# Performance work log

Measured on AMD Instinct MI355X. Metric: run time of the kernel, lower is better.

The kernel has to match this reference:

```python
import jax, jax.numpy as jnp
import numpy as np
import math

N_HEADS = 16
ROPE_BASE = 10000.0


def _rope_interleaved(t, cos, sin):
    # t: [B,H,T,dk]; cos/sin: [T, dk//2] broadcast over B,H
    te, to = t[..., 0::2], t[..., 1::2]
    re = te * cos - to * sin
    ro = te * sin + to * cos
    # interleave back: [..., dk//2, 2] -> [..., dk]
    return jnp.stack([re, ro], axis=-1).reshape(t.shape)


def setup_inputs() -> dict:
    key = jax.random.key(0)
    ks = jax.random.split(key, 5)
    B, T, C = 2, 2048, 1024
    s = 1.0 / math.sqrt(C)
    return {
        "x": jax.random.normal(ks[0], (B, T, C), dtype=jnp.float32),
        "W_qkv": jax.random.normal(ks[1], (C, 3 * C), dtype=jnp.float32) * s,
        "b_qkv": jax.random.normal(ks[2], (3 * C,), dtype=jnp.float32) * 0.02,
        "W_proj": jax.random.normal(ks[3], (C, C), dtype=jnp.float32) * s,
        "b_proj": jax.random.normal(ks[4], (C,), dtype=jnp.float32) * 0.02,
    }


def reference(x, W_qkv, b_qkv, W_proj, b_proj):
    B, T, C = x.shape
    H = N_HEADS
    dk = C // H

    qkv = x @ W_qkv + b_qkv                      # [B,T,3C]
    q, k, v = jnp.split(qkv, 3, axis=-1)
    q = q.reshape(B, T, H, dk).transpose(0, 2, 1, 3)  # [B,H,T,dk]
    k = k.reshape(B, T, H, dk).transpose(0, 2, 1, 3)
    v = v.reshape(B, T, H, dk).transpose(0, 2, 1, 3)

    # RoPE angles: pos * base^(-2i/dk)
    freqs = ROPE_BASE ** (-2.0 * jnp.arange(dk // 2, dtype=jnp.float32) / dk)
    angles = jnp.arange(T, dtype=jnp.float32)[:, None] * freqs[None, :]  # [T,dk//2]
    cos, sin = jnp.cos(angles), jnp.sin(angles)

    q = _rope_interleaved(q, cos, sin)
    k = _rope_interleaved(k, cos, sin)

    attn = jnp.einsum("bhqd,bhkd->bhqk", q, k) / math.sqrt(dk)  # [B,H,T,T]
    causal = jnp.triu(jnp.full((T, T), -jnp.inf, dtype=attn.dtype), k=1)
    attn = jax.nn.softmax(attn + causal, axis=-1)

    scores = jnp.einsum("bhqk,bhkd->bhqd", attn, v)  # [B,H,T,dk]
    scores = scores.transpose(0, 2, 1, 3).reshape(B, T, C)
    return scores @ W_proj + b_proj
```

## Files before the change

### kernel.cpp

```cpp
#include <hip/hip_runtime.h>
#include <hip/hip_bf16.h>

typedef __bf16 bf16x8 __attribute__((ext_vector_type(8)));
typedef float f32x4 __attribute__((ext_vector_type(4)));
typedef float f32x16 __attribute__((ext_vector_type(16)));
typedef unsigned short u16;
typedef u16 u16x8 __attribute__((ext_vector_type(8)));

__device__ __forceinline__ u16 f2bf(float f) {
  union { float f; unsigned u; } v; v.f = f;
  unsigned r = v.u + 0x7fffu + ((v.u >> 16) & 1u);
  return (u16)(r >> 16);
}
__device__ __forceinline__ float bf2f(u16 u) {
  union { unsigned u; float f; } v; v.u = (unsigned)u << 16; return v.f;
}
__device__ __forceinline__ unsigned cvtpk(float a, float b) {
  unsigned r;
  asm("v_cvt_pk_bf16_f32 %0, %1, %2" : "=v"(r) : "v"(a), "v"(b));
  return r;
}
__device__ __forceinline__ float exp2_(float x) {
  float r;
  asm("v_exp_f32 %0, %1" : "=v"(r) : "v"(x));
  return r;
}
__device__ __forceinline__ float sin2pi_(float x) {
  float r;
  asm("v_sin_f32 %0, %1" : "=v"(r) : "v"(x));
  return r;
}
__device__ __forceinline__ float cos2pi_(float x) {
  float r;
  asm("v_cos_f32 %0, %1" : "=v"(r) : "v"(x));
  return r;
}
__device__ __forceinline__ void gload16(const void* g, void* l) {
  __builtin_amdgcn_global_load_lds(
      (__attribute__((address_space(1))) void*)(void*)g,
      (__attribute__((address_space(3))) void*)l, 16, 0, 0);
}

union U8 { bf16x8 v; unsigned u[4]; };

__global__ __launch_bounds__(256) void cast_x_k(const float* __restrict__ x,
                                                u16* __restrict__ xb, int n8) {
  int id = blockIdx.x * 256 + threadIdx.x;
  if (id >= n8) return;
  const float4* p = (const float4*)(x + (size_t)id * 8);
  float4 a = p[0], b = p[1];
  u16x8 o;
  o[0] = f2bf(a.x); o[1] = f2bf(a.y); o[2] = f2bf(a.z); o[3] = f2bf(a.w);
  o[4] = f2bf(b.x); o[5] = f2bf(b.y); o[6] = f2bf(b.z); o[7] = f2bf(b.w);
  *(u16x8*)(xb + (size_t)id * 8) = o;
}

__global__ __launch_bounds__(256) void tcast_k(const float* __restrict__ W,
                                               u16* __restrict__ Wt, int R, int Cc) {
  __shared__ float tile[32][33];
  int bx = blockIdx.x * 32, by = blockIdx.y * 32;
  int tx = threadIdx.x & 31, ty = threadIdx.x >> 5;
#pragma unroll
  for (int j = 0; j < 4; j++)
    tile[ty + j * 8][tx] = W[(size_t)(by + ty + j * 8) * Cc + bx + tx];
  __syncthreads();
#pragma unroll
  for (int j = 0; j < 4; j++)
    Wt[(size_t)(bx + ty + j * 8) * R + by + tx] = f2bf(tile[tx][ty + j * 8]);
}

template <bool BF16OUT>
__global__ __launch_bounds__(256) void gemm_bt_k(const u16* __restrict__ A,
                                                 const u16* __restrict__ Bt,
                                                 const float* __restrict__ bias,
                                                 void* __restrict__ Cv,
                                                 int M, int N, int K) {
  __shared__ u16 As[128 * 64];
  __shared__ u16 Bs[128 * 64];
  int tid = threadIdx.x;
  int m0 = blockIdx.y * 128, n0 = blockIdx.x * 128;
  int wave = tid >> 6, lane = tid & 63;
  int wm = (wave & 1) * 64, wn = (wave >> 1) * 64;
  int lrow = lane & 15, lk = (lane >> 4) * 8;
  int rr = lane >> 3, cb = (lane & 7) * 16;

  f32x4 acc[4][4] = {};

  for (int k0 = 0; k0 < K; k0 += 64) {
#pragma unroll
    for (int i = 0; i < 4; i++) {
      int row = wave * 32 + i * 8 + rr;
      int cc = (cb ^ ((row & 7) << 4)) >> 1;
      gload16(A + (size_t)(m0 + row) * K + k0 + cc, &As[(wave * 32 + i * 8) * 64]);
      gload16(Bt + (size_t)(n0 + row) * K + k0 + cc, &Bs[(wave * 32 + i * 8) * 64]);
    }
    __syncthreads();
#pragma unroll
    for (int kk = 0; kk < 2; kk++) {
      bf16x8 af[4], bfr[4];
#pragma unroll
      for (int i = 0; i < 4; i++) {
        int arow = wm + i * 16 + lrow;
        int ab = (arow * 128 + (kk * 32 + lk) * 2) ^ ((arow & 7) << 4);
        af[i] = *(const bf16x8*)((const char*)As + ab);
        int brow = wn + i * 16 + lrow;
        int bb = (brow * 128 + (kk * 32 + lk) * 2) ^ ((brow & 7) << 4);
        bfr[i] = *(const bf16x8*)((const char*)Bs + bb);
      }
#pragma unroll
      for (int i = 0; i < 4; i++)
#pragma unroll
        for (int j = 0; j < 4; j++)
          acc[i][j] = __builtin_amdgcn_mfma_f32_16x16x32_bf16(af[i], bfr[j], acc[i][j], 0, 0, 0);
    }
    __syncthreads();
  }
  int rg = lane >> 4;
#pragma unroll
  for (int i = 0; i < 4; i++) {
#pragma unroll
    for (int j = 0; j < 4; j++) {
      int col = n0 + wn + j * 16 + lrow;
      float bz = bias ? bias[col] : 0.f;
#pragma unroll
      for (int r = 0; r < 4; r++) {
        int row = m0 + wm + i * 16 + rg * 4 + r;
        float val = acc[i][j][r] + bz;
        if constexpr (BF16OUT)
          ((u16*)Cv)[(size_t)row * N + col] = f2bf(val);
        else
          ((float*)Cv)[(size_t)row * N + col] = val;
      }
    }
  }
}

__global__ __launch_bounds__(256) void rope_pack_k(const u16* __restrict__ qkv,
                                                   u16* __restrict__ qf,
                                                   u16* __restrict__ kf,
                                                   u16* __restrict__ vf) {
  __shared__ u16 tl[64][72];
  int bh = blockIdx.x, tb = blockIdx.y;
  int b = bh >> 4, h = bh & 15;
  int tid = threadIdx.x;
  int tloc = tid >> 2;
  int a = tid & 3;
  int tg = tb * 64 + tloc;
  const u16* rowp = qkv + ((size_t)(b * 2048 + tg)) * 3072 + h * 64 + 16 * a;
  u16x8 q0 = *(const u16x8*)(rowp);
  u16x8 q1 = *(const u16x8*)(rowp + 8);
  u16x8 k0 = *(const u16x8*)(rowp + 1024);
  u16x8 k1 = *(const u16x8*)(rowp + 1032);
  const float QS = 0.18033688011112042f;
  const float C1 = -0.41524101186092029f;
  const float C2 = 0.15915494309189535f;
  u16x8 qo0, qo1, ko0, ko1;
#pragma unroll
  for (int j = 0; j < 8; j++) {
    int i = 8 * a + j;
    float fr = (float)tg * (exp2f((float)i * C1) * C2);
    fr = fr - floorf(fr);
    float sv = sin2pi_(fr), cv = cos2pi_(fr);
    float qx, qy, kx, ky;
    if (j < 4) {
      qx = bf2f(q0[2 * j]); qy = bf2f(q0[2 * j + 1]);
      kx = bf2f(k0[2 * j]); ky = bf2f(k0[2 * j + 1]);
    } else {
      qx = bf2f(q1[2 * j - 8]); qy = bf2f(q1[2 * j - 7]);
      kx = bf2f(k1[2 * j - 8]); ky = bf2f(k1[2 * j - 7]);
    }
    u16 qre = f2bf((qx * cv - qy * sv) * QS), qro = f2bf((qx * sv + qy * cv) * QS);
    u16 kre = f2bf(kx * cv - ky * sv),        kro = f2bf(kx * sv + ky * cv);
    if (j < 4) { qo0[2 * j] = qre; qo0[2 * j + 1] = qro; ko0[2 * j] = kre; ko0[2 * j + 1] = kro; }
    else       { qo1[2 * j - 8] = qre; qo1[2 * j - 7] = qro; ko1[2 * j - 8] = kre; ko1[2 * j - 7] = kro; }
  }
  size_t qbase = ((size_t)bh * 64 + (tg >> 5)) * 2048 + a * 512 + (tg & 31) * 8;
  *(u16x8*)(qf + qbase) = qo0;
  *(u16x8*)(qf + qbase + 256) = qo1;
  size_t kbase = (((size_t)bh * 32 + (tg >> 6)) * 2 + ((tg >> 5) & 1)) * 2048 + a * 512 + (tg & 31) * 8;
  *(u16x8*)(kf + kbase) = ko0;
  *(u16x8*)(kf + kbase + 256) = ko1;
#pragma unroll
  for (int rep = 0; rep < 2; rep++) {
    int tr = rep * 32 + (tid >> 3);
    int dc = (tid & 7) * 8;
    u16x8 v = *(const u16x8*)(qkv + ((size_t)(b * 2048 + tb * 64 + tr)) * 3072 + 2048 + h * 64 + dc);
    *(u16x8*)&tl[tr][dc] = v;
  }
  __syncthreads();
  u16* dst = vf + ((size_t)bh * 32 + tb) * 4096;
#pragma unroll
  for (int rep = 0; rep < 2; rep++) {
    int c = rep * 256 + tid;
    int dh = c >> 8, s = (c >> 6) & 3, l = c & 63;
    int hi = l >> 5, ql = l & 31;
    u16x8 o;
#pragma unroll
    for (int j = 0; j < 8; j++) o[j] = tl[s * 16 + hi * 8 + j][dh * 32 + ql];
    *(u16x8*)(dst + (size_t)c * 8) = o;
  }
}


#define KPREF(K0, K1, IT)                                                         \
  do {                                                                            \
    const u16* kb_ = KfP + (size_t)(IT) * 4096 + ln8;                             \
    _Pragma("unroll") for (int d_ = 0; d_ < 4; d_++) {                            \
      K0[d_] = *(const bf16x8*)(kb_ + d_ * 512);                                  \
      K1[d_] = *(const bf16x8*)(kb_ + 2048 + d_ * 512);                           \
    }                                                                             \
  } while (0)

#define QKC(SA, SB, K0, K1)                                                       \
  do {                                                                            \
    SA = (f32x16){};                                                              \
    SB = (f32x16){};                                                              \
    _Pragma("unroll") for (int d_ = 0; d_ < 4; d_++) {                            \
      SA = __builtin_amdgcn_mfma_f32_32x32x16_bf16(K0[d_], qfr[d_], SA, 0, 0, 0); \
      SB = __builtin_amdgcn_mfma_f32_32x32x16_bf16(K1[d_], qfr[d_], SB, 0, 0, 0); \
    }                                                                             \
  } while (0)

#define VLOADM(IT)                                                                \
  do {                                                                            \
    const u16* vb_ = VfP + (size_t)(IT) * 4096 + ln8;                             \
    _Pragma("unroll") for (int s_ = 0; s_ < 4; s_++) {                            \
      vv0[s_] = *(const bf16x8*)(vb_ + s_ * 512);                                 \
      vv1[s_] = *(const bf16x8*)(vb_ + 2048 + s_ * 512);                          \
    }                                                                             \
  } while (0)

#define SMPV(SA, SB, IT, MASKF)                                                   \
  do {                                                                            \
    if (MASKF) {                                                                  \
      int kv0_ = (IT) * 64;                                                       \
      _Pragma("unroll") for (int r_ = 0; r_ < 16; r_++) {                         \
        int ro_ = (r_ & 3) + 8 * (r_ >> 2) + 4 * hi;                              \
        if (kv0_ + ro_ > qg) SA[r_] = -3e38f;                                     \
        if (kv0_ + 32 + ro_ > qg) SB[r_] = -3e38f;                                \
      }                                                                           \
    }                                                                             \
    _Pragma("unroll") for (int r_ = 0; r_ < 16; r_++) {                           \
      SA[r_] = exp2_(SA[r_]);                                                     \
      SB[r_] = exp2_(SB[r_]);                                                     \
    }                                                                             \
    unsigned w0_ = cvtpk(SA[0], SA[1]),   w1_ = cvtpk(SA[2], SA[3]);              \
    unsigned w2_ = cvtpk(SA[4], SA[5]),   w3_ = cvtpk(SA[6], SA[7]);              \
    unsigned w4_ = cvtpk(SA[8], SA[9]),   w5_ = cvtpk(SA[10], SA[11]);            \
    unsigned w6_ = cvtpk(SA[12], SA[13]), w7_ = cvtpk(SA[14], SA[15]);            \
    unsigned y0_ = cvtpk(SB[0], SB[1]),   y1_ = cvtpk(SB[2], SB[3]);              \
    unsigned y2_ = cvtpk(SB[4], SB[5]),   y3_ = cvtpk(SB[6], SB[7]);              \
    unsigned y4_ = cvtpk(SB[8], SB[9]),   y5_ = cvtpk(SB[10], SB[11]);            \
    unsigned y6_ = cvtpk(SB[12], SB[13]), y7_ = cvtpk(SB[14], SB[15]);            \
    asm("v_permlane32_swap_b32 %0, %1" : "+v"(w0_), "+v"(w2_));                   \
    asm("v_permlane32_swap_b32 %0, %1" : "+v"(w1_), "+v"(w3_));                   \
    asm("v_permlane32_swap_b32 %0, %1" : "+v"(w4_), "+v"(w6_));                   \
    asm("v_permlane32_swap_b32 %0, %1" : "+v"(w5_), "+v"(w7_));                   \
    asm("v_permlane32_swap_b32 %0, %1" : "+v"(y0_), "+v"(y2_));                   \
    asm("v_permlane32_swap_b32 %0, %1" : "+v"(y1_), "+v"(y3_));                   \
    asm("v_permlane32_swap_b32 %0, %1" : "+v"(y4_), "+v"(y6_));                   \
    asm("v_permlane32_swap_b32 %0, %1" : "+v"(y5_), "+v"(y7_));                   \
    U8 pf0_, pf1_, pf2_, pf3_;                                                    \
    pf0_.u[0] = w0_; pf0_.u[1] = w1_; pf0_.u[2] = w2_; pf0_.u[3] = w3_;           \
    pf1_.u[0] = w4_; pf1_.u[1] = w5_; pf1_.u[2] = w6_; pf1_.u[3] = w7_;           \
    pf2_.u[0] = y0_; pf2_.u[1] = y1_; pf2_.u[2] = y2_; pf2_.u[3] = y3_;           \
    pf3_.u[0] = y4_; pf3_.u[1] = y5_; pf3_.u[2] = y6_; pf3_.u[3] = y7_;           \
    o0 = __builtin_amdgcn_mfma_f32_32x32x16_bf16(vv0[0], pf0_.v, o0, 0, 0, 0);    \
    o1 = __builtin_amdgcn_mfma_f32_32x32x16_bf16(vv1[0], pf0_.v, o1, 0, 0, 0);    \
    o0 = __builtin_amdgcn_mfma_f32_32x32x16_bf16(vv0[1], pf1_.v, o0, 0, 0, 0);    \
    o1 = __builtin_amdgcn_mfma_f32_32x32x16_bf16(vv1[1], pf1_.v, o1, 0, 0, 0);    \
    o0 = __builtin_amdgcn_mfma_f32_32x32x16_bf16(vv0[2], pf2_.v, o0, 0, 0, 0);    \
    o1 = __builtin_amdgcn_mfma_f32_32x32x16_bf16(vv1[2], pf2_.v, o1, 0, 0, 0);    \
    o0 = __builtin_amdgcn_mfma_f32_32x32x16_bf16(vv0[3], pf3_.v, o0, 0, 0, 0);    \
    o1 = __builtin_amdgcn_mfma_f32_32x32x16_bf16(vv1[3], pf3_.v, o1, 0, 0, 0);    \
    ls = __builtin_amdgcn_mfma_f32_32x32x16_bf16(onesf.v, pf0_.v, ls, 0, 0, 0);   \
    ls = __builtin_amdgcn_mfma_f32_32x32x16_bf16(onesf.v, pf1_.v, ls, 0, 0, 0);   \
    ls = __builtin_amdgcn_mfma_f32_32x32x16_bf16(onesf.v, pf2_.v, ls, 0, 0, 0);   \
    ls = __builtin_amdgcn_mfma_f32_32x32x16_bf16(onesf.v, pf3_.v, ls, 0, 0, 0);   \
  } while (0)

__global__ __launch_bounds__(64) void attn_k(const u16* __restrict__ Qf,
                                             const u16* __restrict__ Kf,
                                             const u16* __restrict__ Vf,
                                             u16* __restrict__ pO,
                                             float* __restrict__ pL) {
  const int T = 2048;
  int blk = blockIdx.x;
  int bh = (blk & 7) * 4 + ((blk >> 3) & 3);
  int c = blk >> 5;
  int qt, slot;
  if (c < 128)      { qt = 32 + (c >> 2);        slot = c & 3; }
  else if (c < 160) { qt = 16 + ((c - 128) >> 1); slot = (c - 128) & 1; }
  else              { qt = c - 160;               slot = 0; }
  int nTot = (qt >> 1) + 1;
  int nslots = (qt < 16) ? 1 : (qt < 32 ? 2 : 4);
  int it0 = (nTot * slot) / nslots;
  int itEnd = (nTot * (slot + 1)) / nslots;
  int lane = threadIdx.x & 63;
  int ql = lane & 31, hi = lane >> 5;
  int ln8 = lane * 8;
  int qg = qt * 32 + ql;
  const u16* QfP = Qf + (size_t)bh * 64 * 2048;
  const u16* KfP = Kf + (size_t)bh * 32 * 4096;
  const u16* VfP = Vf + (size_t)bh * 32 * 4096;
  int b = bh >> 4, h = bh & 15;

  U8 onesf;
#pragma unroll
  for (int j = 0; j < 4; j++) onesf.u[j] = 0x3F803F80u;

  bf16x8 qfr[4];
#pragma unroll
  for (int ds = 0; ds < 4; ds++)
    qfr[ds] = *(const bf16x8*)(QfP + (size_t)qt * 2048 + ds * 512 + ln8);

  f32x16 o0 = {}, o1 = {}, ls = {};
  bf16x8 Ka0[4], Ka1[4], Kb0[4], Kb1[4], vv0[4], vv1[4];
  f32x16 sA0, sA1, sB0, sB1;

  int t = it0;
  KPREF(Ka0, Ka1, t);
  QKC(sA0, sA1, Ka0, Ka1);
  if (t + 1 < itEnd) KPREF(Kb0, Kb1, t + 1);

  for (;;) {
    bool last = (t == itEnd - 1);
    VLOADM(t);
    if (t + 2 < itEnd) KPREF(Ka0, Ka1, t + 2);
    if (!last) QKC(sB0, sB1, Kb0, Kb1);
    SMPV(sA0, sA1, t, t == nTot - 1);
    if (last) break;
    ++t;
    last = (t == itEnd - 1);
    VLOADM(t);
    if (t + 2 < itEnd) KPREF(Kb0, Kb1, t + 2);
    if (!last) QKC(sA0, sA1, Ka0, Ka1);
    SMPV(sB0, sB1, t, t == nTot - 1);
    if (last) break;
    ++t;
  }

  u16* orow = pO + (size_t)slot * 4194304 + ((size_t)(b * T + qg)) * 1024 + h * 64;
#pragma unroll
  for (int j = 0; j < 4; j++) {
    ushort4 o;
    o.x = f2bf(o0[4 * j + 0]); o.y = f2bf(o0[4 * j + 1]);
    o.z = f2bf(o0[4 * j + 2]); o.w = f2bf(o0[4 * j + 3]);
    *(ushort4*)(orow + 8 * j + 4 * hi) = o;
    ushort4 q2;
    q2.x = f2bf(o1[4 * j + 0]); q2.y = f2bf(o1[4 * j + 1]);
    q2.z = f2bf(o1[4 * j + 2]); q2.w = f2bf(o1[4 * j + 3]);
    *(ushort4*)(orow + 32 + 8 * j + 4 * hi) = q2;
  }
  if (hi == 0) pL[slot * 65536 + bh * 2048 + qg] = ls[0];
}

__global__ __launch_bounds__(256) void mrg_k(const u16* __restrict__ pO,
                                             const float* __restrict__ pL,
                                             u16* __restrict__ sc) {
  int id = blockIdx.x * 256 + threadIdx.x;
  int col8 = id & 127;
  int row = id >> 7;
  int t = row & 2047, b = row >> 11;
  int h = col8 >> 3;
  int qt = t >> 5;
  int ns = (qt < 16) ? 1 : (qt < 32 ? 2 : 4);
  int bh = b * 16 + h;
  float acc[8] = {};
  float lsum = 0.f;
  for (int s = 0; s < ns; s++) {
    lsum += pL[s * 65536 + bh * 2048 + t];
    u16x8 v = *(const u16x8*)(pO + (size_t)s * 4194304 + (size_t)id * 8);
#pragma unroll
    for (int j = 0; j < 8; j++) acc[j] += bf2f(v[j]);
  }
  float inv = 1.f / lsum;
  u16x8 o;
#pragma unroll
  for (int j = 0; j < 8; j++) o[j] = f2bf(acc[j] * inv);
  *(u16x8*)(sc + (size_t)id * 8) = o;
}

extern "C" void kernel_launch(void* const* d_in, const int* in_sizes, int n_in,
                              void* d_out, int out_size, void* d_ws, size_t ws_size,
                              hipStream_t stream) {
  const float* x      = (const float*)d_in[0];
  const float* W_qkv  = (const float*)d_in[1];
  const float* b_qkv  = (const float*)d_in[2];
  const float* W_proj = (const float*)d_in[3];
  const float* b_proj = (const float*)d_in[4];
  float* out = (float*)d_out;

  const int B = 2, T = 2048, C = 1024;
  const int M = B * T;

  char* ws = (char*)d_ws;
  u16* wprojt = (u16*)(ws);
  u16* xb     = (u16*)(ws + (2ull << 20));
  u16* wqkvt  = (u16*)(ws + (10ull << 20));
  u16* qkvb   = (u16*)(ws + (16ull << 20));
  u16* pO     = (u16*)(ws + (2ull << 20));
  float* pL   = (float*)(ws + (34ull << 20));
  u16* qfb    = (u16*)(ws + (40ull << 20));
  u16* kfb    = (u16*)(ws + (48ull << 20));
  u16* vfb    = (u16*)(ws + (56ull << 20));
  u16* sc     = (u16*)(ws + (64ull << 20));

  cast_x_k<<<(M * C / 8 + 255) / 256, 256, 0, stream>>>(x, xb, M * C / 8);
  tcast_k<<<dim3(3 * C / 32, C / 32), 256, 0, stream>>>(W_qkv, wqkvt, C, 3 * C);
  tcast_k<<<dim3(C / 32, C / 32), 256, 0, stream>>>(W_proj, wprojt, C, C);
  gemm_bt_k<true><<<dim3(3 * C / 128, M / 128), 256, 0, stream>>>(xb, wqkvt, b_qkv, qkvb, M, 3 * C, C);
  rope_pack_k<<<dim3(B * 16, T / 64), 256, 0, stream>>>(qkvb, qfb, kfb, vfb);
  attn_k<<<5632, 64, 0, stream>>>(qfb, kfb, vfb, pO, pL);
  mrg_k<<<M * C / 8 / 256, 256, 0, stream>>>(pO, pL, sc);
  gemm_bt_k<false><<<dim3(C / 128, M / 128), 256, 0, stream>>>(sc, wprojt, b_proj, out, M, C, C);
}
```

Baseline: 130.0 us.

## Use 32-key attention tiles, rebalance split-K slots, skip merge for unsplit rows

The attention kernel now walks the causal range in 32-key steps instead of 64-key steps, which cuts masked wasted work on the diagonal. It redistributes query tiles across 4, 3, 2 or 1 split slots to balance per-block work, with a 5120-block grid. Blocks that are not split normalize and write straight to the score buffer, so the merge kernel only handles the split rows (t >= 512). In exchange it drops the double-buffered K prefetch and the overlap of QK and PV across iterations, relying on the occupancy hint (launch_bounds 64,4) to hide load latency instead.

```diff
diff --git a/kernel.cpp b/kernel.cpp
--- a/kernel.cpp
+++ b/kernel.cpp
@@ -201,107 +201,30 @@
   }
 }
 
-
-#define KPREF(K0, K1, IT)                                                         \
-  do {                                                                            \
-    const u16* kb_ = KfP + (size_t)(IT) * 4096 + ln8;                             \
-    _Pragma("unroll") for (int d_ = 0; d_ < 4; d_++) {                            \
-      K0[d_] = *(const bf16x8*)(kb_ + d_ * 512);                                  \
-      K1[d_] = *(const bf16x8*)(kb_ + 2048 + d_ * 512);                           \
-    }                                                                             \
-  } while (0)
-
-#define QKC(SA, SB, K0, K1)                                                       \
-  do {                                                                            \
-    SA = (f32x16){};                                                              \
-    SB = (f32x16){};                                                              \
-    _Pragma("unroll") for (int d_ = 0; d_ < 4; d_++) {                            \
-      SA = __builtin_amdgcn_mfma_f32_32x32x16_bf16(K0[d_], qfr[d_], SA, 0, 0, 0); \
-      SB = __builtin_amdgcn_mfma_f32_32x32x16_bf16(K1[d_], qfr[d_], SB, 0, 0, 0); \
-    }                                                                             \
-  } while (0)
-
-#define VLOADM(IT)                                                                \
-  do {                                                                            \
-    const u16* vb_ = VfP + (size_t)(IT) * 4096 + ln8;                             \
-    _Pragma("unroll") for (int s_ = 0; s_ < 4; s_++) {                            \
-      vv0[s_] = *(const bf16x8*)(vb_ + s_ * 512);                                 \
-      vv1[s_] = *(const bf16x8*)(vb_ + 2048 + s_ * 512);                          \
-    }                                                                             \
-  } while (0)
-
-#define SMPV(SA, SB, IT, MASKF)                                                   \
-  do {                                                                            \
-    if (MASKF) {                                                                  \
-      int kv0_ = (IT) * 64;                                                       \
-      _Pragma("unroll") for (int r_ = 0; r_ < 16; r_++) {                         \
-        int ro_ = (r_ & 3) + 8 * (r_ >> 2) + 4 * hi;                              \
-        if (kv0_ + ro_ > qg) SA[r_] = -3e38f;                                     \
-        if (kv0_ + 32 + ro_ > qg) SB[r_] = -3e38f;                                \
-      }                                                                           \
-    }                                                                             \
-    _Pragma("unroll") for (int r_ = 0; r_ < 16; r_++) {                           \
-      SA[r_] = exp2_(SA[r_]);                                                     \
-      SB[r_] = exp2_(SB[r_]);                                                     \
-    }                                                                             \
-    unsigned w0_ = cvtpk(SA[0], SA[1]),   w1_ = cvtpk(SA[2], SA[3]);              \
-    unsigned w2_ = cvtpk(SA[4], SA[5]),   w3_ = cvtpk(SA[6], SA[7]);              \
-    unsigned w4_ = cvtpk(SA[8], SA[9]),   w5_ = cvtpk(SA[10], SA[11]);            \
-    unsigned w6_ = cvtpk(SA[12], SA[13]), w7_ = cvtpk(SA[14], SA[15]);            \
-    unsigned y0_ = cvtpk(SB[0], SB[1]),   y1_ = cvtpk(SB[2], SB[3]);              \
-    unsigned y2_ = cvtpk(SB[4], SB[5]),   y3_ = cvtpk(SB[6], SB[7]);              \
-    unsigned y4_ = cvtpk(SB[8], SB[9]),   y5_ = cvtpk(SB[10], SB[11]);            \
-    unsigned y6_ = cvtpk(SB[12], SB[13]), y7_ = cvtpk(SB[14], SB[15]);            \
-    asm("v_permlane32_swap_b32 %0, %1" : "+v"(w0_), "+v"(w2_));                   \
-    asm("v_permlane32_swap_b32 %0, %1" : "+v"(w1_), "+v"(w3_));                   \
-    asm("v_permlane32_swap_b32 %0, %1" : "+v"(w4_), "+v"(w6_));                   \
-    asm("v_permlane32_swap_b32 %0, %1" : "+v"(w5_), "+v"(w7_));                   \
-    asm("v_permlane32_swap_b32 %0, %1" : "+v"(y0_), "+v"(y2_));                   \
-    asm("v_permlane32_swap_b32 %0, %1" : "+v"(y1_), "+v"(y3_));                   \
-    asm("v_permlane32_swap_b32 %0, %1" : "+v"(y4_), "+v"(y6_));                   \
-    asm("v_permlane32_swap_b32 %0, %1" : "+v"(y5_), "+v"(y7_));                   \
-    U8 pf0_, pf1_, pf2_, pf3_;                                                    \
-    pf0_.u[0] = w0_; pf0_.u[1] = w1_; pf0_.u[2] = w2_; pf0_.u[3] = w3_;           \
-    pf1_.u[0] = w4_; pf1_.u[1] = w5_; pf1_.u[2] = w6_; pf1_.u[3] = w7_;           \
-    pf2_.u[0] = y0_; pf2_.u[1] = y1_; pf2_.u[2] = y2_; pf2_.u[3] = y3_;           \
-    pf3_.u[0] = y4_; pf3_.u[1] = y5_; pf3_.u[2] = y6_; pf3_.u[3] = y7_;           \
-    o0 = __builtin_amdgcn_mfma_f32_32x32x16_bf16(vv0[0], pf0_.v, o0, 0, 0, 0);    \
-    o1 = __builtin_amdgcn_mfma_f32_32x32x16_bf16(vv1[0], pf0_.v, o1, 0, 0, 0);    \
-    o0 = __builtin_amdgcn_mfma_f32_32x32x16_bf16(vv0[1], pf1_.v, o0, 0, 0, 0);    \
-    o1 = __builtin_amdgcn_mfma_f32_32x32x16_bf16(vv1[1], pf1_.v, o1, 0, 0, 0);    \
-    o0 = __builtin_amdgcn_mfma_f32_32x32x16_bf16(vv0[2], pf2_.v, o0, 0, 0, 0);    \
-    o1 = __builtin_amdgcn_mfma_f32_32x32x16_bf16(vv1[2], pf2_.v, o1, 0, 0, 0);    \
-    o0 = __builtin_amdgcn_mfma_f32_32x32x16_bf16(vv0[3], pf3_.v, o0, 0, 0, 0);    \
-    o1 = __builtin_amdgcn_mfma_f32_32x32x16_bf16(vv1[3], pf3_.v, o1, 0, 0, 0);    \
-    ls = __builtin_amdgcn_mfma_f32_32x32x16_bf16(onesf.v, pf0_.v, ls, 0, 0, 0);   \
-    ls = __builtin_amdgcn_mfma_f32_32x32x16_bf16(onesf.v, pf1_.v, ls, 0, 0, 0);   \
-    ls = __builtin_amdgcn_mfma_f32_32x32x16_bf16(onesf.v, pf2_.v, ls, 0, 0, 0);   \
-    ls = __builtin_amdgcn_mfma_f32_32x32x16_bf16(onesf.v, pf3_.v, ls, 0, 0, 0);   \
-  } while (0)
-
-__global__ __launch_bounds__(64) void attn_k(const u16* __restrict__ Qf,
-                                             const u16* __restrict__ Kf,
-                                             const u16* __restrict__ Vf,
-                                             u16* __restrict__ pO,
-                                             float* __restrict__ pL) {
+__global__ __launch_bounds__(64, 4) void attn_k(const u16* __restrict__ Qf,
+                                                const u16* __restrict__ Kf,
+                                                const u16* __restrict__ Vf,
+                                                u16* __restrict__ sc,
+                                                u16* __restrict__ pO,
+                                                float* __restrict__ pL) {
   const int T = 2048;
   int blk = blockIdx.x;
   int bh = (blk & 7) * 4 + ((blk >> 3) & 3);
   int c = blk >> 5;
-  int qt, slot;
-  if (c < 128)      { qt = 32 + (c >> 2);        slot = c & 3; }
-  else if (c < 160) { qt = 16 + ((c - 128) >> 1); slot = (c - 128) & 1; }
-  else              { qt = c - 160;               slot = 0; }
-  int nTot = (qt >> 1) + 1;
-  int nslots = (qt < 16) ? 1 : (qt < 32 ? 2 : 4);
-  int it0 = (nTot * slot) / nslots;
-  int itEnd = (nTot * (slot + 1)) / nslots;
+  int qt, slot, nslots;
+  if (c < 64)       { qt = 63 - (c >> 2);              slot = c & 3;        nslots = 4; }
+  else if (c < 112) { int cc = c - 64; int d3 = cc / 3; qt = 47 - d3;       slot = cc - 3 * d3; nslots = 3; }
+  else if (c < 144) { int cc = c - 112; qt = 31 - (cc >> 1); slot = cc & 1; nslots = 2; }
+  else              { qt = 159 - c;                    slot = 0;            nslots = 1; }
+  int nIter = qt + 1;
+  int it0 = (nIter * slot) / nslots;
+  int itEnd = (nIter * (slot + 1)) / nslots;
   int lane = threadIdx.x & 63;
   int ql = lane & 31, hi = lane >> 5;
   int ln8 = lane * 8;
   int qg = qt * 32 + ql;
   const u16* QfP = Qf + (size_t)bh * 64 * 2048;
-  const u16* KfP = Kf + (size_t)bh * 32 * 4096;
+  const u16* KfP = Kf + (size_t)bh * 64 * 2048;
   const u16* VfP = Vf + (size_t)bh * 32 * 4096;
   int b = bh >> 4, h = bh & 15;
 
@@ -315,44 +238,81 @@
     qfr[ds] = *(const bf16x8*)(QfP + (size_t)qt * 2048 + ds * 512 + ln8);
 
   f32x16 o0 = {}, o1 = {}, ls = {};
-  bf16x8 Ka0[4], Ka1[4], Kb0[4], Kb1[4], vv0[4], vv1[4];
-  f32x16 sA0, sA1, sB0, sB1;
-
-  int t = it0;
-  KPREF(Ka0, Ka1, t);
-  QKC(sA0, sA1, Ka0, Ka1);
-  if (t + 1 < itEnd) KPREF(Kb0, Kb1, t + 1);
-
-  for (;;) {
-    bool last = (t == itEnd - 1);
-    VLOADM(t);
-    if (t + 2 < itEnd) KPREF(Ka0, Ka1, t + 2);
-    if (!last) QKC(sB0, sB1, Kb0, Kb1);
-    SMPV(sA0, sA1, t, t == nTot - 1);
-    if (last) break;
-    ++t;
-    last = (t == itEnd - 1);
-    VLOADM(t);
-    if (t + 2 < itEnd) KPREF(Kb0, Kb1, t + 2);
-    if (!last) QKC(sA0, sA1, Ka0, Ka1);
-    SMPV(sB0, sB1, t, t == nTot - 1);
-    if (last) break;
-    ++t;
-  }
-
-  u16* orow = pO + (size_t)slot * 4194304 + ((size_t)(b * T + qg)) * 1024 + h * 64;
-#pragma unroll
-  for (int j = 0; j < 4; j++) {
-    ushort4 o;
-    o.x = f2bf(o0[4 * j + 0]); o.y = f2bf(o0[4 * j + 1]);
-    o.z = f2bf(o0[4 * j + 2]); o.w = f2bf(o0[4 * j + 3]);
-    *(ushort4*)(orow + 8 * j + 4 * hi) = o;
-    ushort4 q2;
-    q2.x = f2bf(o1[4 * j + 0]); q2.y = f2bf(o1[4 * j + 1]);
-    q2.z = f2bf(o1[4 * j + 2]); q2.w = f2bf(o1[4 * j + 3]);
-    *(ushort4*)(orow + 32 + 8 * j + 4 * hi) = q2;
-  }
-  if (hi == 0) pL[slot * 65536 + bh * 2048 + qg] = ls[0];
+
+  for (int t = it0; t < itEnd; ++t) {
+    const u16* kb = KfP + (size_t)t * 2048 + ln8;
+    bf16x8 k0 = *(const bf16x8*)(kb);
+    bf16x8 k1 = *(const bf16x8*)(kb + 512);
+    bf16x8 k2 = *(const bf16x8*)(kb + 1024);
+    bf16x8 k3 = *(const bf16x8*)(kb + 1536);
+    f32x16 S = {};
+    S = __builtin_amdgcn_mfma_f32_32x32x16_bf16(k0, qfr[0], S, 0, 0, 0);
+    S = __builtin_amdgcn_mfma_f32_32x32x16_bf16(k1, qfr[1], S, 0, 0, 0);
+    S = __builtin_amdgcn_mfma_f32_32x32x16_bf16(k2, qfr[2], S, 0, 0, 0);
+    S = __builtin_amdgcn_mfma_f32_32x32x16_bf16(k3, qfr[3], S, 0, 0, 0);
+    const u16* vb = VfP + (size_t)(t >> 1) * 4096 + (t & 1) * 1024 + ln8;
+    bf16x8 v00 = *(const bf16x8*)(vb);
+    bf16x8 v01 = *(const bf16x8*)(vb + 512);
+    bf16x8 v10 = *(const bf16x8*)(vb + 2048);
+    bf16x8 v11 = *(const bf16x8*)(vb + 2560);
+    if (t == nIter - 1) {
+      int kv0 = t * 32;
+#pragma unroll
+      for (int r = 0; r < 16; r++) {
+        int k = kv0 + ((r & 3) + 8 * (r >> 2) + 4 * hi);
+        if (k > qg) S[r] = -3e38f;
+      }
+    }
+#pragma unroll
+    for (int r = 0; r < 16; r++) S[r] = exp2_(S[r]);
+    unsigned w0 = cvtpk(S[0], S[1]),   w1 = cvtpk(S[2], S[3]);
+    unsigned w2 = cvtpk(S[4], S[5]),   w3 = cvtpk(S[6], S[7]);
+    unsigned w4 = cvtpk(S[8], S[9]),   w5 = cvtpk(S[10], S[11]);
+    unsigned w6 = cvtpk(S[12], S[13]), w7 = cvtpk(S[14], S[15]);
+    asm("v_permlane32_swap_b32 %0, %1" : "+v"(w0), "+v"(w2));
+    asm("v_permlane32_swap_b32 %0, %1" : "+v"(w1), "+v"(w3));
+    asm("v_permlane32_swap_b32 %0, %1" : "+v"(w4), "+v"(w6));
+    asm("v_permlane32_swap_b32 %0, %1" : "+v"(w5), "+v"(w7));
+    U8 pf0, pf1;
+    pf0.u[0] = w0; pf0.u[1] = w1; pf0.u[2] = w2; pf0.u[3] = w3;
+    pf1.u[0] = w4; pf1.u[1] = w5; pf1.u[2] = w6; pf1.u[3] = w7;
+    o0 = __builtin_amdgcn_mfma_f32_32x32x16_bf16(v00, pf0.v, o0, 0, 0, 0);
+    o0 = __builtin_amdgcn_mfma_f32_32x32x16_bf16(v01, pf1.v, o0, 0, 0, 0);
+    o1 = __builtin_amdgcn_mfma_f32_32x32x16_bf16(v10, pf0.v, o1, 0, 0, 0);
+    o1 = __builtin_amdgcn_mfma_f32_32x32x16_bf16(v11, pf1.v, o1, 0, 0, 0);
+    ls = __builtin_amdgcn_mfma_f32_32x32x16_bf16(onesf.v, pf0.v, ls, 0, 0, 0);
+    ls = __builtin_amdgcn_mfma_f32_32x32x16_bf16(onesf.v, pf1.v, ls, 0, 0, 0);
+  }
+
+  if (nslots == 1) {
+    float inv = 1.f / ls[0];
+    u16* orow = sc + ((size_t)(b * T + qg)) * 1024 + h * 64;
+#pragma unroll
+    for (int j = 0; j < 4; j++) {
+      ushort4 o;
+      o.x = f2bf(o0[4 * j + 0] * inv); o.y = f2bf(o0[4 * j + 1] * inv);
+      o.z = f2bf(o0[4 * j + 2] * inv); o.w = f2bf(o0[4 * j + 3] * inv);
+      *(ushort4*)(orow + 8 * j + 4 * hi) = o;
+      ushort4 q2;
+      q2.x = f2bf(o1[4 * j + 0] * inv); q2.y = f2bf(o1[4 * j + 1] * inv);
+      q2.z = f2bf(o1[4 * j + 2] * inv); q2.w = f2bf(o1[4 * j + 3] * inv);
+      *(ushort4*)(orow + 32 + 8 * j + 4 * hi) = q2;
+    }
+  } else {
+    u16* orow = pO + (size_t)slot * 4194304 + ((size_t)(b * T + qg)) * 1024 + h * 64;
+#pragma unroll
+    for (int j = 0; j < 4; j++) {
+      ushort4 o;
+      o.x = f2bf(o0[4 * j + 0]); o.y = f2bf(o0[4 * j + 1]);
+      o.z = f2bf(o0[4 * j + 2]); o.w = f2bf(o0[4 * j + 3]);
+      *(ushort4*)(orow + 8 * j + 4 * hi) = o;
+      ushort4 q2;
+      q2.x = f2bf(o1[4 * j + 0]); q2.y = f2bf(o1[4 * j + 1]);
+      q2.z = f2bf(o1[4 * j + 2]); q2.w = f2bf(o1[4 * j + 3]);
+      *(ushort4*)(orow + 32 + 8 * j + 4 * hi) = q2;
+    }
+    if (hi == 0) pL[slot * 65536 + bh * 2048 + qg] = ls[0];
+  }
 }
 
 __global__ __launch_bounds__(256) void mrg_k(const u16* __restrict__ pO,
@@ -360,17 +320,19 @@
                                              u16* __restrict__ sc) {
   int id = blockIdx.x * 256 + threadIdx.x;
   int col8 = id & 127;
-  int row = id >> 7;
-  int t = row & 2047, b = row >> 11;
+  int rp = id >> 7;
+  int b = (rp >= 1536) ? 1 : 0;
+  int t = 512 + rp - b * 1536;
   int h = col8 >> 3;
   int qt = t >> 5;
-  int ns = (qt < 16) ? 1 : (qt < 32 ? 2 : 4);
+  int ns = (qt >= 48) ? 4 : (qt >= 32) ? 3 : 2;
   int bh = b * 16 + h;
+  size_t idx8 = ((size_t)(b * 2048 + t) * 128 + col8);
   float acc[8] = {};
   float lsum = 0.f;
   for (int s = 0; s < ns; s++) {
     lsum += pL[s * 65536 + bh * 2048 + t];
-    u16x8 v = *(const u16x8*)(pO + (size_t)s * 4194304 + (size_t)id * 8);
+    u16x8 v = *(const u16x8*)(pO + (size_t)s * 4194304 + idx8 * 8);
 #pragma unroll
     for (int j = 0; j < 8; j++) acc[j] += bf2f(v[j]);
   }
@@ -378,7 +340,7 @@
   u16x8 o;
 #pragma unroll
   for (int j = 0; j < 8; j++) o[j] = f2bf(acc[j] * inv);
-  *(u16x8*)(sc + (size_t)id * 8) = o;
+  *(u16x8*)(sc + idx8 * 8) = o;
 }
 
 extern "C" void kernel_launch(void* const* d_in, const int* in_sizes, int n_in,
@@ -411,7 +373,7 @@
   tcast_k<<<dim3(C / 32, C / 32), 256, 0, stream>>>(W_proj, wprojt, C, C);
   gemm_bt_k<true><<<dim3(3 * C / 128, M / 128), 256, 0, stream>>>(xb, wqkvt, b_qkv, qkvb, M, 3 * C, C);
   rope_pack_k<<<dim3(B * 16, T / 64), 256, 0, stream>>>(qkvb, qfb, kfb, vfb);
-  attn_k<<<5632, 64, 0, stream>>>(qfb, kfb, vfb, pO, pL);
-  mrg_k<<<M * C / 8 / 256, 256, 0, stream>>>(pO, pL, sc);
+  attn_k<<<5120, 64, 0, stream>>>(qfb, kfb, vfb, sc, pO, pL);
+  mrg_k<<<1536, 256, 0, stream>>>(pO, pL, sc);
   gemm_bt_k<false><<<dim3(C / 128, M / 128), 256, 0, stream>>>(sc, wprojt, b_proj, out, M, C, C);
 }
```

Result: faster. 121.2 us (-6.8%).

## Reduce attention split-K to two slots for late tiles and normalize in-kernel

Applied to the files above, without the earlier changes.

Changes the attention work split so only the last 16 query tiles (qt 48-63) are split into two KV slots, and all other tiles run unsplit, longest tiles first. Unsplit tiles now normalize by the row sum and write final bf16 output directly, so the merge kernel only runs over the 512 rows per batch that were split. This cuts partial-output traffic and merge work and shrinks the grid from 5632 to 2560 blocks. In exchange there is less parallelism, and long unsplit tiles in the middle range may leave the tail of the launch unbalanced.

```diff
diff --git a/kernel.cpp b/kernel.cpp
--- a/kernel.cpp
+++ b/kernel.cpp
@@ -282,18 +282,17 @@
 __global__ __launch_bounds__(64) void attn_k(const u16* __restrict__ Qf,
                                              const u16* __restrict__ Kf,
                                              const u16* __restrict__ Vf,
+                                             u16* __restrict__ sc,
                                              u16* __restrict__ pO,
                                              float* __restrict__ pL) {
   const int T = 2048;
   int blk = blockIdx.x;
   int bh = (blk & 7) * 4 + ((blk >> 3) & 3);
   int c = blk >> 5;
-  int qt, slot;
-  if (c < 128)      { qt = 32 + (c >> 2);        slot = c & 3; }
-  else if (c < 160) { qt = 16 + ((c - 128) >> 1); slot = (c - 128) & 1; }
-  else              { qt = c - 160;               slot = 0; }
+  int qt, slot, nslots;
+  if (c < 32) { qt = 63 - (c >> 1); slot = c & 1; nslots = 2; }
+  else        { qt = 79 - c;        slot = 0;     nslots = 1; }
   int nTot = (qt >> 1) + 1;
-  int nslots = (qt < 16) ? 1 : (qt < 32 ? 2 : 4);
   int it0 = (nTot * slot) / nslots;
   int itEnd = (nTot * (slot + 1)) / nslots;
   int lane = threadIdx.x & 63;
@@ -340,19 +339,35 @@
     ++t;
   }
 
-  u16* orow = pO + (size_t)slot * 4194304 + ((size_t)(b * T + qg)) * 1024 + h * 64;
-#pragma unroll
-  for (int j = 0; j < 4; j++) {
-    ushort4 o;
-    o.x = f2bf(o0[4 * j + 0]); o.y = f2bf(o0[4 * j + 1]);
-    o.z = f2bf(o0[4 * j + 2]); o.w = f2bf(o0[4 * j + 3]);
-    *(ushort4*)(orow + 8 * j + 4 * hi) = o;
-    ushort4 q2;
-    q2.x = f2bf(o1[4 * j + 0]); q2.y = f2bf(o1[4 * j + 1]);
-    q2.z = f2bf(o1[4 * j + 2]); q2.w = f2bf(o1[4 * j + 3]);
-    *(ushort4*)(orow + 32 + 8 * j + 4 * hi) = q2;
-  }
-  if (hi == 0) pL[slot * 65536 + bh * 2048 + qg] = ls[0];
+  if (nslots == 1) {
+    float inv = 1.f / ls[0];
+    u16* orow = sc + ((size_t)(b * T + qg)) * 1024 + h * 64;
+#pragma unroll
+    for (int j = 0; j < 4; j++) {
+      ushort4 o;
+      o.x = f2bf(o0[4 * j + 0] * inv); o.y = f2bf(o0[4 * j + 1] * inv);
+      o.z = f2bf(o0[4 * j + 2] * inv); o.w = f2bf(o0[4 * j + 3] * inv);
+      *(ushort4*)(orow + 8 * j + 4 * hi) = o;
+      ushort4 q2;
+      q2.x = f2bf(o1[4 * j + 0] * inv); q2.y = f2bf(o1[4 * j + 1] * inv);
+      q2.z = f2bf(o1[4 * j + 2] * inv); q2.w = f2bf(o1[4 * j + 3] * inv);
+      *(ushort4*)(orow + 32 + 8 * j + 4 * hi) = q2;
+    }
+  } else {
+    u16* orow = pO + (size_t)slot * 4194304 + ((size_t)(b * T + qg)) * 1024 + h * 64;
+#pragma unroll
+    for (int j = 0; j < 4; j++) {
+      ushort4 o;
+      o.x = f2bf(o0[4 * j + 0]); o.y = f2bf(o0[4 * j + 1]);
+      o.z = f2bf(o0[4 * j + 2]); o.w = f2bf(o0[4 * j + 3]);
+      *(ushort4*)(orow + 8 * j + 4 * hi) = o;
+      ushort4 q2;
+      q2.x = f2bf(o1[4 * j + 0]); q2.y = f2bf(o1[4 * j + 1]);
+      q2.z = f2bf(o1[4 * j + 2]); q2.w = f2bf(o1[4 * j + 3]);
+      *(ushort4*)(orow + 32 + 8 * j + 4 * hi) = q2;
+    }
+    if (hi == 0) pL[slot * 65536 + bh * 2048 + qg] = ls[0];
+  }
 }
 
 __global__ __launch_bounds__(256) void mrg_k(const u16* __restrict__ pO,
@@ -360,25 +375,21 @@
                                              u16* __restrict__ sc) {
   int id = blockIdx.x * 256 + threadIdx.x;
   int col8 = id & 127;
-  int row = id >> 7;
-  int t = row & 2047, b = row >> 11;
+  int rp = id >> 7;
+  int b = rp >> 9;
+  int t = 1536 + (rp & 511);
   int h = col8 >> 3;
-  int qt = t >> 5;
-  int ns = (qt < 16) ? 1 : (qt < 32 ? 2 : 4);
   int bh = b * 16 + h;
-  float acc[8] = {};
-  float lsum = 0.f;
-  for (int s = 0; s < ns; s++) {
-    lsum += pL[s * 65536 + bh * 2048 + t];
-    u16x8 v = *(const u16x8*)(pO + (size_t)s * 4194304 + (size_t)id * 8);
-#pragma unroll
-    for (int j = 0; j < 8; j++) acc[j] += bf2f(v[j]);
-  }
-  float inv = 1.f / lsum;
+  size_t idx8 = ((size_t)(b * 2048 + t) * 128 + col8);
+  float l0 = pL[bh * 2048 + t];
+  float l1 = pL[65536 + bh * 2048 + t];
+  u16x8 v0 = *(const u16x8*)(pO + idx8 * 8);
+  u16x8 v1 = *(const u16x8*)(pO + 4194304 + idx8 * 8);
+  float inv = 1.f / (l0 + l1);
   u16x8 o;
 #pragma unroll
-  for (int j = 0; j < 8; j++) o[j] = f2bf(acc[j] * inv);
-  *(u16x8*)(sc + (size_t)id * 8) = o;
+  for (int j = 0; j < 8; j++) o[j] = f2bf((bf2f(v0[j]) + bf2f(v1[j])) * inv);
+  *(u16x8*)(sc + idx8 * 8) = o;
 }
 
 extern "C" void kernel_launch(void* const* d_in, const int* in_sizes, int n_in,
@@ -411,7 +422,7 @@
   tcast_k<<<dim3(C / 32, C / 32), 256, 0, stream>>>(W_proj, wprojt, C, C);
   gemm_bt_k<true><<<dim3(3 * C / 128, M / 128), 256, 0, stream>>>(xb, wqkvt, b_qkv, qkvb, M, 3 * C, C);
   rope_pack_k<<<dim3(B * 16, T / 64), 256, 0, stream>>>(qkvb, qfb, kfb, vfb);
-  attn_k<<<5632, 64, 0, stream>>>(qfb, kfb, vfb, pO, pL);
-  mrg_k<<<M * C / 8 / 256, 256, 0, stream>>>(pO, pL, sc);
+  attn_k<<<2560, 64, 0, stream>>>(qfb, kfb, vfb, sc, pO, pL);
+  mrg_k<<<512, 256, 0, stream>>>(pO, pL, sc);
   gemm_bt_k<false><<<dim3(C / 128, M / 128), 256, 0, stream>>>(sc, wprojt, b_proj, out, M, C, C);
 }
```

Result: faster. 118.5 us (-8.8%).
